# Kernel tuning notes

Hardware: AMD Instinct MI355X
Metric: run time of the kernel (lower is better)

The kernel has to match this reference:

```python
import jax, jax.numpy as jnp
import numpy as np

N_HEADS = 16
D_MODEL = 1024
DEPTH = D_MODEL // N_HEADS
B, S = 2, 2048


def setup_inputs() -> dict:
    key = jax.random.key(0)
    ks = jax.random.split(key, 12)
    sc = 1.0 / np.sqrt(D_MODEL)
    inp = {
        "q": jax.random.normal(ks[0], (B, S, D_MODEL), jnp.float32),
        "k": jax.random.normal(ks[1], (B, S, D_MODEL), jnp.float32),
        "v": jax.random.normal(ks[2], (B, S, D_MODEL), jnp.float32),
        "mask": (jax.random.uniform(ks[3], (B, 1, 1, S)) < 0.1).astype(jnp.float32),
        "Wq": jax.random.normal(ks[4], (D_MODEL, D_MODEL), jnp.float32) * sc,
        "bq": jnp.zeros((D_MODEL,), jnp.float32),
        "Wk": jax.random.normal(ks[5], (D_MODEL, D_MODEL), jnp.float32) * sc,
        "bk": jnp.zeros((D_MODEL,), jnp.float32),
        "Wv": jax.random.normal(ks[6], (D_MODEL, D_MODEL), jnp.float32) * sc,
        "bv": jnp.zeros((D_MODEL,), jnp.float32),
        "Wo": jax.random.normal(ks[7], (D_MODEL, D_MODEL), jnp.float32) * sc,
        "bo": jnp.zeros((D_MODEL,), jnp.float32),
    }
    return inp


def _split_heads(x):
    b, s, _ = x.shape
    return x.reshape(b, s, N_HEADS, DEPTH).transpose(0, 2, 1, 3)  # [b,h,s,d]


def reference(q, k, v, mask, Wq, bq, Wk, bk, Wv, bv, Wo, bo):
    qh = _split_heads(q @ Wq + bq)
    kh = _split_heads(k @ Wk + bk)
    vh = _split_heads(v @ Wv + bv)
    inv_sqrt_dk = 1.0 / jnp.sqrt(jnp.float32(DEPTH))
    scores = jnp.einsum("bhqd,bhkd->bhqk", qh, kh) * inv_sqrt_dk
    att_weight = jax.nn.softmax(scores, axis=-1)
    # NOTE: faithful to source — mask is added AFTER softmax
    att_weight = att_weight + mask * (-1e9)
    ctx = jnp.einsum("bhqk,bhkd->bhqd", att_weight, vh)
    b = q.shape[0]
    concat = ctx.transpose(0, 2, 1, 3).reshape(b, -1, D_MODEL)
    output = concat @ Wo + bo
    return output, att_weight
```

## Files before the change

### kernel.cpp

```cpp
#include <hip/hip_runtime.h>

typedef unsigned short u16;
typedef short bf16x8 __attribute__((ext_vector_type(8)));
typedef float f32x4 __attribute__((ext_vector_type(4)));

#define MFMA16(a, b, c) __builtin_amdgcn_mfma_f32_16x16x32_bf16((a), (b), (c), 0, 0, 0)

__device__ __forceinline__ u16 f2bf(float f) {
  union { float f; unsigned u; } v; v.f = f;
  unsigned r = v.u + 0x7fffu + ((v.u >> 16) & 1u);
  return (u16)(r >> 16);
}
__device__ __forceinline__ float bf2f(u16 u) {
  union { unsigned u; float f; } v; v.u = ((unsigned)u) << 16;
  return v.f;
}

__global__ __launch_bounds__(256) void convert_qkv(
    const float* __restrict__ q, const float* __restrict__ k, const float* __restrict__ v,
    u16* __restrict__ qb, u16* __restrict__ kb, u16* __restrict__ vb) {
  const int t = blockIdx.x * 256 + threadIdx.x;
  const float* src = (blockIdx.y == 0) ? q : (blockIdx.y == 1) ? k : v;
  u16* dst = (blockIdx.y == 0) ? qb : (blockIdx.y == 1) ? kb : vb;
  float4 f = ((const float4*)src)[t];
  ushort4 u;
  u.x = f2bf(f.x); u.y = f2bf(f.y); u.z = f2bf(f.z); u.w = f2bf(f.w);
  ((ushort4*)dst)[t] = u;
}

__global__ __launch_bounds__(256) void transpose_w(
    const float* __restrict__ W0, const float* __restrict__ W1,
    const float* __restrict__ W2, const float* __restrict__ W3,
    u16* __restrict__ T0, u16* __restrict__ T1, u16* __restrict__ T2, u16* __restrict__ T3) {
  __shared__ float tile[64][65];
  const float* W = (blockIdx.y == 0) ? W0 : (blockIdx.y == 1) ? W1 : (blockIdx.y == 2) ? W2 : W3;
  u16* T = (blockIdx.y == 0) ? T0 : (blockIdx.y == 1) ? T1 : (blockIdx.y == 2) ? T2 : T3;
  const int bx = blockIdx.x;
  const int kt = (bx >> 4) * 64, nt = (bx & 15) * 64;
  const int t = threadIdx.x;
#pragma unroll
  for (int i = 0; i < 16; ++i) {
    int e = t + i * 256, r = e >> 6, c = e & 63;
    tile[r][c] = W[(size_t)(kt + r) * 1024 + nt + c];
  }
  __syncthreads();
#pragma unroll
  for (int i = 0; i < 16; ++i) {
    int e = t + i * 256, rn = e >> 6, ck = e & 63;
    T[(size_t)(nt + rn) * 1024 + kt + ck] = f2bf(tile[ck][rn]);
  }
}

template <int MODE>
__global__ __launch_bounds__(256) void gemm_bt(
    const u16* __restrict__ A, const u16* __restrict__ Bt,
    const float* __restrict__ bias, void* __restrict__ dstv) {
  __shared__ __align__(16) u16 As[128 * 72];
  __shared__ __align__(16) u16 Bs[128 * 72];
  const int tid = threadIdx.x;
  const int wv = tid >> 6, lane = tid & 63, quad = lane >> 4, l16 = lane & 15;
  const int wq = wv >> 1, wn = wv & 1;
  const int m0 = blockIdx.y * 128, n0 = blockIdx.x * 128;

  f32x4 acc[4][4] = {};

  for (int kt = 0; kt < 16; ++kt) {
    const int k0 = kt * 64;
    __syncthreads();
#pragma unroll
    for (int i = 0; i < 4; ++i) {
      int e = tid + i * 256, r = e >> 3, c8 = (e & 7) << 3;
      *(uint4*)(&As[r * 72 + c8]) = *(const uint4*)(A + (size_t)(m0 + r) * 1024 + k0 + c8);
      *(uint4*)(&Bs[r * 72 + c8]) = *(const uint4*)(Bt + (size_t)(n0 + r) * 1024 + k0 + c8);
    }
    __syncthreads();
#pragma unroll
    for (int kk = 0; kk < 2; ++kk) {
      bf16x8 af[4], bf[4];
#pragma unroll
      for (int mi = 0; mi < 4; ++mi)
        af[mi] = *(const bf16x8*)(&As[(wq * 64 + mi * 16 + l16) * 72 + kk * 32 + quad * 8]);
#pragma unroll
      for (int ni = 0; ni < 4; ++ni)
        bf[ni] = *(const bf16x8*)(&Bs[(wn * 64 + ni * 16 + l16) * 72 + kk * 32 + quad * 8]);
#pragma unroll
      for (int mi = 0; mi < 4; ++mi)
#pragma unroll
        for (int ni = 0; ni < 4; ++ni)
          acc[mi][ni] = MFMA16(af[mi], bf[ni], acc[mi][ni]);
    }
  }
#pragma unroll
  for (int ni = 0; ni < 4; ++ni) {
    const int col = n0 + wn * 64 + ni * 16 + l16;
    const float bv = bias[col];
#pragma unroll
    for (int mi = 0; mi < 4; ++mi) {
#pragma unroll
      for (int r = 0; r < 4; ++r) {
        const int row = m0 + wq * 64 + mi * 16 + quad * 4 + r;
        const float val = acc[mi][ni][r] + bv;
        if (MODE == 2) {
          ((float*)dstv)[(size_t)row * 1024 + col] = val;
        } else {
          const int bb = row >> 11, s = row & 2047, h = col >> 6, dh = col & 63;
          if (MODE == 0)
            ((u16*)dstv)[((size_t)((bb << 4) + h) * 2048 + s) * 64 + dh] = f2bf(val);
          else
            ((u16*)dstv)[((size_t)((bb << 4) + h) * 64 + dh) * 2048 + s] = f2bf(val);
        }
      }
    }
  }
}

__global__ __launch_bounds__(256, 2) void attn_fused(
    const u16* __restrict__ qh, const u16* __restrict__ kh, const u16* __restrict__ vhT,
    const float* __restrict__ maskg, float* __restrict__ attg, u16* __restrict__ ctx) {
  __shared__ __align__(16) u16 Qs[64 * 72];
  __shared__ __align__(16) u16 Ks[128 * 72];
  __shared__ __align__(16) u16 Vs[64 * 136];
  __shared__ __align__(16) u16 Ps[64 * 136];
  __shared__ float msk[128];
  __shared__ float lpart[4][64];

  const int tid = threadIdx.x;
  const int wv = tid >> 6, lane = tid & 63, quad = lane >> 4, l16 = lane & 15;
  const int bx = blockIdx.x, bh = bx >> 5, qi = bx & 31;
  const int b = bh >> 4, h = bh & 15;
  const int q0 = qi * 64;

  {
    const u16* qsrc = qh + ((size_t)bh * 2048 + q0) * 64;
#pragma unroll
    for (int i = 0; i < 2; ++i) {
      int e = tid + i * 256, r = e >> 3, c8 = (e & 7) << 3;
      *(uint4*)(&Qs[r * 72 + c8]) = *(const uint4*)(qsrc + r * 64 + c8);
    }
  }

  float l_acc[4][4] = {};
  for (int c = 0; c < 16; ++c) {
    __syncthreads();
    const u16* ksrc = kh + ((size_t)bh * 2048 + c * 128) * 64;
#pragma unroll
    for (int i = 0; i < 4; ++i) {
      int e = tid + i * 256, r = e >> 3, c8 = (e & 7) << 3;
      *(uint4*)(&Ks[r * 72 + c8]) = *(const uint4*)(ksrc + r * 64 + c8);
    }
    __syncthreads();
    f32x4 s[4][2] = {};
#pragma unroll
    for (int kk = 0; kk < 2; ++kk) {
      bf16x8 af[4], bf[2];
#pragma unroll
      for (int mi = 0; mi < 4; ++mi)
        af[mi] = *(const bf16x8*)(&Qs[(mi * 16 + l16) * 72 + kk * 32 + quad * 8]);
#pragma unroll
      for (int ni = 0; ni < 2; ++ni)
        bf[ni] = *(const bf16x8*)(&Ks[(wv * 32 + ni * 16 + l16) * 72 + kk * 32 + quad * 8]);
#pragma unroll
      for (int mi = 0; mi < 4; ++mi)
#pragma unroll
        for (int ni = 0; ni < 2; ++ni)
          s[mi][ni] = MFMA16(af[mi], bf[ni], s[mi][ni]);
    }
#pragma unroll
    for (int mi = 0; mi < 4; ++mi)
#pragma unroll
      for (int r = 0; r < 4; ++r)
        l_acc[mi][r] += __expf(s[mi][0][r] * 0.125f) + __expf(s[mi][1][r] * 0.125f);
  }
#pragma unroll
  for (int mi = 0; mi < 4; ++mi)
#pragma unroll
    for (int r = 0; r < 4; ++r) {
      float v = l_acc[mi][r];
      v += __shfl_xor(v, 1); v += __shfl_xor(v, 2);
      v += __shfl_xor(v, 4); v += __shfl_xor(v, 8);
      l_acc[mi][r] = v;
    }
  if (l16 == 0) {
#pragma unroll
    for (int mi = 0; mi < 4; ++mi)
#pragma unroll
      for (int r = 0; r < 4; ++r) lpart[wv][mi * 16 + quad * 4 + r] = l_acc[mi][r];
  }
  __syncthreads();
  float inv_l[4][4];
#pragma unroll
  for (int mi = 0; mi < 4; ++mi)
#pragma unroll
    for (int r = 0; r < 4; ++r) {
      int row = mi * 16 + quad * 4 + r;
      inv_l[mi][r] = 1.0f / (lpart[0][row] + lpart[1][row] + lpart[2][row] + lpart[3][row]);
    }

  f32x4 o[4] = {};
  for (int c = 0; c < 16; ++c) {
    __syncthreads();
    {
      const u16* ksrc = kh + ((size_t)bh * 2048 + c * 128) * 64;
#pragma unroll
      for (int i = 0; i < 4; ++i) {
        int e = tid + i * 256, r = e >> 3, c8 = (e & 7) << 3;
        *(uint4*)(&Ks[r * 72 + c8]) = *(const uint4*)(ksrc + r * 64 + c8);
      }
      const u16* vsrc = vhT + (size_t)bh * 64 * 2048 + c * 128;
#pragma unroll
      for (int i = 0; i < 4; ++i) {
        int e = tid + i * 256, d = e >> 4, cu = (e & 15) << 3;
        *(uint4*)(&Vs[d * 136 + cu]) = *(const uint4*)(vsrc + (size_t)d * 2048 + cu);
      }
      if (tid < 128) msk[tid] = maskg[(size_t)b * 2048 + c * 128 + tid];
    }
    __syncthreads();
    f32x4 s[4][2] = {};
#pragma unroll
    for (int kk = 0; kk < 2; ++kk) {
      bf16x8 af[4], bf[2];
#pragma unroll
      for (int mi = 0; mi < 4; ++mi)
        af[mi] = *(const bf16x8*)(&Qs[(mi * 16 + l16) * 72 + kk * 32 + quad * 8]);
#pragma unroll
      for (int ni = 0; ni < 2; ++ni)
        bf[ni] = *(const bf16x8*)(&Ks[(wv * 32 + ni * 16 + l16) * 72 + kk * 32 + quad * 8]);
#pragma unroll
      for (int mi = 0; mi < 4; ++mi)
#pragma unroll
        for (int ni = 0; ni < 2; ++ni)
          s[mi][ni] = MFMA16(af[mi], bf[ni], s[mi][ni]);
    }
#pragma unroll
    for (int mi = 0; mi < 4; ++mi)
#pragma unroll
      for (int ni = 0; ni < 2; ++ni) {
        const float mval = msk[wv * 32 + ni * 16 + l16];
#pragma unroll
        for (int r = 0; r < 4; ++r) {
          float p = __expf(s[mi][ni][r] * 0.125f) * inv_l[mi][r];
          Ps[(mi * 16 + quad * 4 + r) * 136 + wv * 32 + ni * 16 + l16] = f2bf(p - 1e9f * mval);
        }
      }
    __syncthreads();
#pragma unroll
    for (int kk = 0; kk < 4; ++kk) {
      bf16x8 bf = *(const bf16x8*)(&Vs[(wv * 16 + l16) * 136 + kk * 32 + quad * 8]);
#pragma unroll
      for (int mi = 0; mi < 4; ++mi) {
        bf16x8 af = *(const bf16x8*)(&Ps[(mi * 16 + l16) * 136 + kk * 32 + quad * 8]);
        o[mi] = MFMA16(af, bf, o[mi]);
      }
    }
    float* adst = attg + ((size_t)bh * 2048 + q0) * 2048 + c * 128;
#pragma unroll
    for (int i = 0; i < 4; ++i) {
      int e = tid + i * 256, r = e >> 4, cu = (e & 15) << 3;
      uint4 pv = *(const uint4*)(&Ps[r * 136 + cu]);
      const u16* pu = (const u16*)&pv;
      float4 w0 = make_float4(bf2f(pu[0]), bf2f(pu[1]), bf2f(pu[2]), bf2f(pu[3]));
      float4 w1 = make_float4(bf2f(pu[4]), bf2f(pu[5]), bf2f(pu[6]), bf2f(pu[7]));
      *(float4*)(adst + (size_t)r * 2048 + cu) = w0;
      *(float4*)(adst + (size_t)r * 2048 + cu + 4) = w1;
    }
  }
#pragma unroll
  for (int mi = 0; mi < 4; ++mi)
#pragma unroll
    for (int r = 0; r < 4; ++r) {
      int row = mi * 16 + quad * 4 + r;
      ctx[((size_t)(b * 2048 + q0 + row)) * 1024 + h * 64 + wv * 16 + l16] = f2bf(o[mi][r]);
    }
}

extern "C" void kernel_launch(void* const* d_in, const int* in_sizes, int n_in,
                              void* d_out, int out_size, void* d_ws, size_t ws_size,
                              hipStream_t stream) {
  (void)in_sizes; (void)n_in; (void)out_size; (void)ws_size;
  const float* q = (const float*)d_in[0];
  const float* k = (const float*)d_in[1];
  const float* v = (const float*)d_in[2];
  const float* mask = (const float*)d_in[3];
  const float* Wq = (const float*)d_in[4];
  const float* bq = (const float*)d_in[5];
  const float* Wk = (const float*)d_in[6];
  const float* bk = (const float*)d_in[7];
  const float* Wv = (const float*)d_in[8];
  const float* bv = (const float*)d_in[9];
  const float* Wo = (const float*)d_in[10];
  const float* bo = (const float*)d_in[11];

  float* out = (float*)d_out;
  float* attg = out + (size_t)4194304;

  u16* ws = (u16*)d_ws;
  u16* qb = ws;
  u16* kb = qb + (1u << 22);
  u16* vb = kb + (1u << 22);
  u16* WqT = vb + (1u << 22);
  u16* WkT = WqT + (1u << 20);
  u16* WvT = WkT + (1u << 20);
  u16* WoT = WvT + (1u << 20);
  u16* qhp = WoT + (1u << 20);
  u16* khp = qhp + (1u << 22);
  u16* vhT = khp + (1u << 22);
  u16* ctx = vhT + (1u << 22);

  convert_qkv<<<dim3(4096, 3), 256, 0, stream>>>(q, k, v, qb, kb, vb);
  transpose_w<<<dim3(256, 4), 256, 0, stream>>>(Wq, Wk, Wv, Wo, WqT, WkT, WvT, WoT);
  gemm_bt<0><<<dim3(8, 32), 256, 0, stream>>>(qb, WqT, bq, qhp);
  gemm_bt<0><<<dim3(8, 32), 256, 0, stream>>>(kb, WkT, bk, khp);
  gemm_bt<1><<<dim3(8, 32), 256, 0, stream>>>(vb, WvT, bv, vhT);
  attn_fused<<<dim3(1024), 256, 0, stream>>>(qhp, khp, vhT, mask, attg, ctx);
  gemm_bt<2><<<dim3(8, 32), 256, 0, stream>>>(ctx, WoT, bo, out);
}
```

Baseline: 812.6 us.

## Use direct global-to-LDS loads with XOR swizzle and batch QKV GEMMs

```diff
diff --git a/kernel.cpp b/kernel.cpp
--- a/kernel.cpp
+++ b/kernel.cpp
@@ -14,6 +14,12 @@
 __device__ __forceinline__ float bf2f(u16 u) {
   union { unsigned u; float f; } v; v.u = ((unsigned)u) << 16;
   return v.f;
+}
+
+__device__ __forceinline__ void load_lds16(const u16* g, u16* l) {
+  __builtin_amdgcn_global_load_lds(
+      (const __attribute__((address_space(1))) unsigned int*)g,
+      (__attribute__((address_space(3))) unsigned int*)l, 16, 0, 0);
 }
 
 __global__ __launch_bounds__(256) void convert_qkv(
@@ -51,40 +57,52 @@
   }
 }
 
-template <int MODE>
-__global__ __launch_bounds__(256) void gemm_bt(
+template <int BM>
+__device__ __forceinline__ void gemm_core(
     const u16* __restrict__ A, const u16* __restrict__ Bt,
-    const float* __restrict__ bias, void* __restrict__ dstv) {
-  __shared__ __align__(16) u16 As[128 * 72];
-  __shared__ __align__(16) u16 Bs[128 * 72];
+    const float* __restrict__ bias, void* __restrict__ dstv, const int mode) {
+  constexpr int WM = BM / 2;
+  constexpr int MI = WM / 16;
+  constexpr int LA = BM / 32;
+  __shared__ __align__(16) u16 As[BM * 64];
+  __shared__ __align__(16) u16 Bs[128 * 64];
   const int tid = threadIdx.x;
   const int wv = tid >> 6, lane = tid & 63, quad = lane >> 4, l16 = lane & 15;
   const int wq = wv >> 1, wn = wv & 1;
-  const int m0 = blockIdx.y * 128, n0 = blockIdx.x * 128;
-
-  f32x4 acc[4][4] = {};
+  const int m0 = blockIdx.y * BM, n0 = blockIdx.x * 128;
+
+  f32x4 acc[MI][4] = {};
 
   for (int kt = 0; kt < 16; ++kt) {
     const int k0 = kt * 64;
     __syncthreads();
 #pragma unroll
+    for (int i = 0; i < LA; ++i) {
+      const int e = tid + i * 256, r = e >> 3, g = e & 7;
+      load_lds16(A + (size_t)(m0 + r) * 1024 + k0 + ((g ^ (r & 7)) << 3), &As[e * 8]);
+    }
+#pragma unroll
     for (int i = 0; i < 4; ++i) {
-      int e = tid + i * 256, r = e >> 3, c8 = (e & 7) << 3;
-      *(uint4*)(&As[r * 72 + c8]) = *(const uint4*)(A + (size_t)(m0 + r) * 1024 + k0 + c8);
-      *(uint4*)(&Bs[r * 72 + c8]) = *(const uint4*)(Bt + (size_t)(n0 + r) * 1024 + k0 + c8);
+      const int e = tid + i * 256, r = e >> 3, g = e & 7;
+      load_lds16(Bt + (size_t)(n0 + r) * 1024 + k0 + ((g ^ (r & 7)) << 3), &Bs[e * 8]);
     }
     __syncthreads();
 #pragma unroll
     for (int kk = 0; kk < 2; ++kk) {
-      bf16x8 af[4], bf[4];
-#pragma unroll
-      for (int mi = 0; mi < 4; ++mi)
-        af[mi] = *(const bf16x8*)(&As[(wq * 64 + mi * 16 + l16) * 72 + kk * 32 + quad * 8]);
-#pragma unroll
-      for (int ni = 0; ni < 4; ++ni)
-        bf[ni] = *(const bf16x8*)(&Bs[(wn * 64 + ni * 16 + l16) * 72 + kk * 32 + quad * 8]);
-#pragma unroll
-      for (int mi = 0; mi < 4; ++mi)
+      bf16x8 af[MI], bf[4];
+      const int ce = kk * 32 + quad * 8;
+#pragma unroll
+      for (int mi = 0; mi < MI; ++mi) {
+        const int row = wq * WM + mi * 16 + l16;
+        af[mi] = *(const bf16x8*)(&As[row * 64 + (ce ^ ((row & 7) << 3))]);
+      }
+#pragma unroll
+      for (int ni = 0; ni < 4; ++ni) {
+        const int row = wn * 64 + ni * 16 + l16;
+        bf[ni] = *(const bf16x8*)(&Bs[row * 64 + (ce ^ ((row & 7) << 3))]);
+      }
+#pragma unroll
+      for (int mi = 0; mi < MI; ++mi)
 #pragma unroll
         for (int ni = 0; ni < 4; ++ni)
           acc[mi][ni] = MFMA16(af[mi], bf[ni], acc[mi][ni]);
@@ -95,16 +113,16 @@
     const int col = n0 + wn * 64 + ni * 16 + l16;
     const float bv = bias[col];
 #pragma unroll
-    for (int mi = 0; mi < 4; ++mi) {
+    for (int mi = 0; mi < MI; ++mi) {
 #pragma unroll
       for (int r = 0; r < 4; ++r) {
-        const int row = m0 + wq * 64 + mi * 16 + quad * 4 + r;
+        const int row = m0 + wq * WM + mi * 16 + quad * 4 + r;
         const float val = acc[mi][ni][r] + bv;
-        if (MODE == 2) {
+        if (mode == 2) {
           ((float*)dstv)[(size_t)row * 1024 + col] = val;
         } else {
           const int bb = row >> 11, s = row & 2047, h = col >> 6, dh = col & 63;
-          if (MODE == 0)
+          if (mode == 0)
             ((u16*)dstv)[((size_t)((bb << 4) + h) * 2048 + s) * 64 + dh] = f2bf(val);
           else
             ((u16*)dstv)[((size_t)((bb << 4) + h) * 64 + dh) * 2048 + s] = f2bf(val);
@@ -114,12 +132,31 @@
   }
 }
 
+__global__ __launch_bounds__(256, 2) void gemm_qkv(
+    const u16* __restrict__ qb, const u16* __restrict__ kb, const u16* __restrict__ vb,
+    const u16* __restrict__ WqT, const u16* __restrict__ WkT, const u16* __restrict__ WvT,
+    const float* __restrict__ bq, const float* __restrict__ bk, const float* __restrict__ bv,
+    u16* __restrict__ qhp, u16* __restrict__ khp, u16* __restrict__ vhT) {
+  const int z = blockIdx.z;
+  const u16* A = (z == 0) ? qb : (z == 1) ? kb : vb;
+  const u16* Bt = (z == 0) ? WqT : (z == 1) ? WkT : WvT;
+  const float* bias = (z == 0) ? bq : (z == 1) ? bk : bv;
+  void* dst = (z == 0) ? (void*)qhp : (z == 1) ? (void*)khp : (void*)vhT;
+  gemm_core<128>(A, Bt, bias, dst, (z == 2) ? 1 : 0);
+}
+
+__global__ __launch_bounds__(256, 2) void gemm_o(
+    const u16* __restrict__ ctx, const u16* __restrict__ WoT,
+    const float* __restrict__ bo, float* __restrict__ out) {
+  gemm_core<64>(ctx, WoT, bo, (void*)out, 2);
+}
+
 __global__ __launch_bounds__(256, 2) void attn_fused(
     const u16* __restrict__ qh, const u16* __restrict__ kh, const u16* __restrict__ vhT,
     const float* __restrict__ maskg, float* __restrict__ attg, u16* __restrict__ ctx) {
-  __shared__ __align__(16) u16 Qs[64 * 72];
-  __shared__ __align__(16) u16 Ks[128 * 72];
-  __shared__ __align__(16) u16 Vs[64 * 136];
+  __shared__ __align__(16) u16 Qs[64 * 64];
+  __shared__ __align__(16) u16 Ks[128 * 64];
+  __shared__ __align__(16) u16 Vs[64 * 128];
   __shared__ __align__(16) u16 Ps[64 * 136];
   __shared__ float msk[128];
   __shared__ float lpart[4][64];
@@ -134,8 +171,8 @@
     const u16* qsrc = qh + ((size_t)bh * 2048 + q0) * 64;
 #pragma unroll
     for (int i = 0; i < 2; ++i) {
-      int e = tid + i * 256, r = e >> 3, c8 = (e & 7) << 3;
-      *(uint4*)(&Qs[r * 72 + c8]) = *(const uint4*)(qsrc + r * 64 + c8);
+      int e = tid + i * 256, r = e >> 3, g = e & 7;
+      *(uint4*)(&Qs[r * 64 + ((g ^ (r & 7)) << 3)]) = *(const uint4*)(qsrc + r * 64 + (g << 3));
     }
   }
 
@@ -145,20 +182,25 @@
     const u16* ksrc = kh + ((size_t)bh * 2048 + c * 128) * 64;
 #pragma unroll
     for (int i = 0; i < 4; ++i) {
-      int e = tid + i * 256, r = e >> 3, c8 = (e & 7) << 3;
-      *(uint4*)(&Ks[r * 72 + c8]) = *(const uint4*)(ksrc + r * 64 + c8);
+      int e = tid + i * 256, r = e >> 3, g = e & 7;
+      load_lds16(ksrc + r * 64 + ((g ^ (r & 7)) << 3), &Ks[e * 8]);
     }
     __syncthreads();
     f32x4 s[4][2] = {};
 #pragma unroll
     for (int kk = 0; kk < 2; ++kk) {
       bf16x8 af[4], bf[2];
-#pragma unroll
-      for (int mi = 0; mi < 4; ++mi)
-        af[mi] = *(const bf16x8*)(&Qs[(mi * 16 + l16) * 72 + kk * 32 + quad * 8]);
-#pragma unroll
-      for (int ni = 0; ni < 2; ++ni)
-        bf[ni] = *(const bf16x8*)(&Ks[(wv * 32 + ni * 16 + l16) * 72 + kk * 32 + quad * 8]);
+      const int ce = kk * 32 + quad * 8;
+#pragma unroll
+      for (int mi = 0; mi < 4; ++mi) {
+        const int row = mi * 16 + l16;
+        af[mi] = *(const bf16x8*)(&Qs[row * 64 + (ce ^ ((row & 7) << 3))]);
+      }
+#pragma unroll
+      for (int ni = 0; ni < 2; ++ni) {
+        const int row = wv * 32 + ni * 16 + l16;
+        bf[ni] = *(const bf16x8*)(&Ks[row * 64 + (ce ^ ((row & 7) << 3))]);
+      }
 #pragma unroll
       for (int mi = 0; mi < 4; ++mi)
 #pragma unroll
@@ -203,14 +245,14 @@
       const u16* ksrc = kh + ((size_t)bh * 2048 + c * 128) * 64;
 #pragma unroll
       for (int i = 0; i < 4; ++i) {
-        int e = tid + i * 256, r = e >> 3, c8 = (e & 7) << 3;
-        *(uint4*)(&Ks[r * 72 + c8]) = *(const uint4*)(ksrc + r * 64 + c8);
+        int e = tid + i * 256, r = e >> 3, g = e & 7;
+        load_lds16(ksrc + r * 64 + ((g ^ (r & 7)) << 3), &Ks[e * 8]);
       }
       const u16* vsrc = vhT + (size_t)bh * 64 * 2048 + c * 128;
 #pragma unroll
       for (int i = 0; i < 4; ++i) {
-        int e = tid + i * 256, d = e >> 4, cu = (e & 15) << 3;
-        *(uint4*)(&Vs[d * 136 + cu]) = *(const uint4*)(vsrc + (size_t)d * 2048 + cu);
+        int e = tid + i * 256, d = e >> 4, g = e & 15;
+        load_lds16(vsrc + (size_t)d * 2048 + ((g ^ (d & 15)) << 3), &Vs[e * 8]);
       }
       if (tid < 128) msk[tid] = maskg[(size_t)b * 2048 + c * 128 + tid];
     }
@@ -219,12 +261,17 @@
 #pragma unroll
     for (int kk = 0; kk < 2; ++kk) {
       bf16x8 af[4], bf[2];
-#pragma unroll
-      for (int mi = 0; mi < 4; ++mi)
-        af[mi] = *(const bf16x8*)(&Qs[(mi * 16 + l16) * 72 + kk * 32 + quad * 8]);
-#pragma unroll
-      for (int ni = 0; ni < 2; ++ni)
-        bf[ni] = *(const bf16x8*)(&Ks[(wv * 32 + ni * 16 + l16) * 72 + kk * 32 + quad * 8]);
+      const int ce = kk * 32 + quad * 8;
+#pragma unroll
+      for (int mi = 0; mi < 4; ++mi) {
+        const int row = mi * 16 + l16;
+        af[mi] = *(const bf16x8*)(&Qs[row * 64 + (ce ^ ((row & 7) << 3))]);
+      }
+#pragma unroll
+      for (int ni = 0; ni < 2; ++ni) {
+        const int row = wv * 32 + ni * 16 + l16;
+        bf[ni] = *(const bf16x8*)(&Ks[row * 64 + (ce ^ ((row & 7) << 3))]);
+      }
 #pragma unroll
       for (int mi = 0; mi < 4; ++mi)
 #pragma unroll
@@ -245,11 +292,12 @@
     __syncthreads();
 #pragma unroll
     for (int kk = 0; kk < 4; ++kk) {
-      bf16x8 bf = *(const bf16x8*)(&Vs[(wv * 16 + l16) * 136 + kk * 32 + quad * 8]);
+      const int ce = kk * 32 + quad * 8;
+      bf16x8 bfv = *(const bf16x8*)(&Vs[(wv * 16 + l16) * 128 + (ce ^ (l16 << 3))]);
 #pragma unroll
       for (int mi = 0; mi < 4; ++mi) {
         bf16x8 af = *(const bf16x8*)(&Ps[(mi * 16 + l16) * 136 + kk * 32 + quad * 8]);
-        o[mi] = MFMA16(af, bf, o[mi]);
+        o[mi] = MFMA16(af, bfv, o[mi]);
       }
     }
     float* adst = attg + ((size_t)bh * 2048 + q0) * 2048 + c * 128;
@@ -308,9 +356,7 @@
 
   convert_qkv<<<dim3(4096, 3), 256, 0, stream>>>(q, k, v, qb, kb, vb);
   transpose_w<<<dim3(256, 4), 256, 0, stream>>>(Wq, Wk, Wv, Wo, WqT, WkT, WvT, WoT);
-  gemm_bt<0><<<dim3(8, 32), 256, 0, stream>>>(qb, WqT, bq, qhp);
-  gemm_bt<0><<<dim3(8, 32), 256, 0, stream>>>(kb, WkT, bk, khp);
-  gemm_bt<1><<<dim3(8, 32), 256, 0, stream>>>(vb, WvT, bv, vhT);
+  gemm_qkv<<<dim3(8, 32, 3), 256, 0, stream>>>(qb, kb, vb, WqT, WkT, WvT, bq, bk, bv, qhp, khp, vhT);
   attn_fused<<<dim3(1024), 256, 0, stream>>>(qhp, khp, vhT, mask, attg, ctx);
-  gemm_bt<2><<<dim3(8, 32), 256, 0, stream>>>(ctx, WoT, bo, out);
-}
+  gemm_o<<<dim3(8, 64), 256, 0, stream>>>(ctx, WoT, bo, out);
+}
```

Measured after the change: 767.5 us. 1.06x faster.
